# Kernel tuning notes

Hardware: AMD Instinct MI355X
Metric: run time of the kernel (lower is better)

Reference implementation:

```python
import jax, jax.numpy as jnp
import numpy as np

D_MODEL = 2048
D_COMPARE = 2048
D_MEMORY = 2048
N_HEADS = 16
KV_HEADS = 4
KV_REPEAT = N_HEADS // KV_HEADS          # 4
C_HD = D_COMPARE // N_HEADS              # 128 compare head dim
M_HD = D_MEMORY // N_HEADS               # 128 memory head dim
TOTAL_OUT = D_COMPARE + KV_HEADS * C_HD + KV_HEADS * M_HD  # 3072


def setup_inputs() -> dict:
    key = jax.random.key(0)
    ks = jax.random.split(key, 5)
    b, t = 2, 2048
    x = jax.random.normal(ks[0], (b, t, D_MODEL), dtype=jnp.float32)
    s_in = 1.0 / np.sqrt(D_MODEL)
    s_out = 1.0 / np.sqrt(D_MEMORY)
    in_w = jax.random.uniform(ks[1], (TOTAL_OUT, D_MODEL), jnp.float32, -s_in, s_in)
    in_b = jax.random.uniform(ks[2], (TOTAL_OUT,), jnp.float32, -s_in, s_in)
    out_w = jax.random.uniform(ks[3], (D_MODEL, D_MEMORY), jnp.float32, -s_out, s_out)
    out_b = jax.random.uniform(ks[4], (D_MODEL,), jnp.float32, -s_out, s_out)
    return {"x": x, "in_w": in_w, "in_b": in_b, "out_w": out_w, "out_b": out_b}


def reference(x, in_w, in_b, out_w, out_b):
    b, t, _ = x.shape
    packed = jnp.einsum("btd,od->bto", x, in_w) + in_b          # [b,t,TOTAL_OUT]
    q, k, v = jnp.split(packed, [D_COMPARE, D_COMPARE + KV_HEADS * C_HD], axis=-1)
    # q: [b, kv, rep, t, hd] -- head h maps to kv group h // KV_REPEAT
    # (torch repeat_interleave on KV head dim == grouped reshape of q heads)
    q = q.reshape(b, t, KV_HEADS, KV_REPEAT, C_HD).transpose(0, 2, 3, 1, 4)
    k = k.reshape(b, t, KV_HEADS, C_HD).transpose(0, 2, 1, 3)   # [b,kv,t,hd]
    v = v.reshape(b, t, KV_HEADS, M_HD).transpose(0, 2, 1, 3)   # [b,kv,t,mhd]
    scale = 1.0 / np.sqrt(C_HD)
    scores = jnp.einsum("bgrqd,bgkd->bgrqk", q, k) * scale      # [b,kv,rep,t,t]
    attn = jax.nn.softmax(scores, axis=-1)
    y = jnp.einsum("bgrqk,bgkd->bgrqd", attn, v)                # [b,kv,rep,t,mhd]
    y = y.transpose(0, 3, 1, 2, 4).reshape(b, t, D_MEMORY)      # heads back in order
    return jnp.einsum("btm,dm->btd", y, out_w) + out_b
```

## Files before the change

kernel.cpp:

```cpp
#include <hip/hip_runtime.h>
#include <hip/hip_bf16.h>
#include <stdint.h>

#define DEV __device__ __forceinline__

typedef __attribute__((ext_vector_type(8))) short bf16x8;
typedef __attribute__((ext_vector_type(4))) float f32x4;

DEV unsigned short f2bf(float f) {
  unsigned u = __builtin_bit_cast(unsigned, f);
  unsigned r = u + 0x7FFF + ((u >> 16) & 1);
  return (unsigned short)(r >> 16);
}

typedef __attribute__((address_space(1))) void gvoid;
typedef __attribute__((address_space(3))) void lvoid;

DEV void g2l16(const void* g, void* l) {
  __builtin_amdgcn_global_load_lds((gvoid*)g, (lvoid*)l, 16, 0, 0);
}

#define MFMA16(a, b, c) __builtin_amdgcn_mfma_f32_16x16x32_bf16(a, b, c, 0, 0, 0)

__global__ void k_cvt(const float* __restrict__ in, unsigned short* __restrict__ out, int n4) {
  int i = blockIdx.x * blockDim.x + threadIdx.x;
  int stride = gridDim.x * blockDim.x;
  for (; i < n4; i += stride) {
    float4 v = reinterpret_cast<const float4*>(in)[i];
    ushort4 o;
    o.x = f2bf(v.x); o.y = f2bf(v.y); o.z = f2bf(v.z); o.w = f2bf(v.w);
    reinterpret_cast<ushort4*>(out)[i] = o;
  }
}

template<bool BF16OUT>
__global__ __launch_bounds__(256, 2) void k_gemm(
    const unsigned short* __restrict__ A, const unsigned short* __restrict__ B,
    const float* __restrict__ bias, void* __restrict__ C,
    int M, int N, int K) {
  __shared__ unsigned short As[128 * 32];
  __shared__ unsigned short Bs[128 * 32];
  int tid = threadIdx.x;
  int lane = tid & 63, wid = tid >> 6;
  int bm = blockIdx.y * 128, bn = blockIdx.x * 128;
  int wm = (wid >> 1) * 64, wn = (wid & 1) * 64;
  int row16 = lane & 15, kq = lane >> 4;
  f32x4 acc[4][4] = {};
  int r = tid >> 2, c = (tid & 3) * 8;
  const unsigned short* Ag = A + (size_t)(bm + r) * K + c;
  const unsigned short* Bg = B + (size_t)(bn + r) * K + c;
  for (int k0 = 0; k0 < K; k0 += 32) {
    g2l16(Ag + k0, &As[tid * 8]);
    g2l16(Ag + (size_t)64 * K + k0, &As[2048 + tid * 8]);
    g2l16(Bg + k0, &Bs[tid * 8]);
    g2l16(Bg + (size_t)64 * K + k0, &Bs[2048 + tid * 8]);
    __syncthreads();
    bf16x8 a[4], b[4];
#pragma unroll
    for (int m = 0; m < 4; m++) a[m] = *(const bf16x8*)&As[(wm + m * 16 + row16) * 32 + kq * 8];
#pragma unroll
    for (int n = 0; n < 4; n++) b[n] = *(const bf16x8*)&Bs[(wn + n * 16 + row16) * 32 + kq * 8];
    __builtin_amdgcn_s_setprio(1);
#pragma unroll
    for (int m = 0; m < 4; m++)
#pragma unroll
      for (int n = 0; n < 4; n++)
        acc[m][n] = MFMA16(a[m], b[n], acc[m][n]);
    __builtin_amdgcn_s_setprio(0);
    __syncthreads();
  }
#pragma unroll
  for (int n = 0; n < 4; n++) {
    int col = bn + wn + n * 16 + row16;
    float bv = bias[col];
#pragma unroll
    for (int m = 0; m < 4; m++) {
      int rw = bm + wm + m * 16 + kq * 4;
#pragma unroll
      for (int j = 0; j < 4; j++) {
        float v = acc[m][n][j] + bv;
        if (BF16OUT) ((unsigned short*)C)[(size_t)(rw + j) * N + col] = f2bf(v);
        else         ((float*)C)[(size_t)(rw + j) * N + col] = v;
      }
    }
  }
}

__global__ void k_vt(const unsigned short* __restrict__ packed, unsigned short* __restrict__ vT) {
  __shared__ unsigned short tile[64][136];
  int g = blockIdx.y;
  int b = g >> 2, kv = g & 3;
  int t0 = blockIdx.x * 64;
  int tid = threadIdx.x;
#pragma unroll
  for (int i = 0; i < 4; i++) {
    int tl = i * 16 + (tid >> 4);
    int d0 = (tid & 15) * 8;
    bf16x8 v = *(const bf16x8*)&packed[(size_t)(b * 2048 + t0 + tl) * 3072 + 2560 + kv * 128 + d0];
    *(bf16x8*)&tile[tl][d0] = v;
  }
  __syncthreads();
  int d = tid >> 1, ts = (tid & 1) * 32;
  size_t obase = (size_t)(g * 128 + d) * 2048 + t0 + ts;
#pragma unroll
  for (int j = 0; j < 4; j++) {
    bf16x8 o;
#pragma unroll
    for (int e = 0; e < 8; e++) o[e] = (short)tile[ts + j * 8 + e][d];
    *(bf16x8*)&vT[obase + j * 8] = o;
  }
}

__global__ __launch_bounds__(256, 2) void k_flash(
    const unsigned short* __restrict__ packed,
    const unsigned short* __restrict__ vT,
    unsigned short* __restrict__ Y) {
  __shared__ unsigned short Ks[2][64 * 128];
  __shared__ unsigned short Vs[128 * 64];
  __shared__ unsigned short Ps[4][2][16 * 68];
  __shared__ float Axc[4][2][16];
  int tid = threadIdx.x, lane = tid & 63, wid = tid >> 6;
  int row16 = lane & 15, kq = lane >> 4;
  int r3 = row16 & 7;
  int g = blockIdx.x;
  int s8 = g & 7;
  int b = s8 >> 2, kv = s8 & 3;
  int w = g >> 3;
  int h = kv * 4 + (w & 3);
  int qt = w >> 2;
  size_t prow = (size_t)b * 2048;

  unsigned short* Q = &Ks[0][0];
  {
    int rr = tid >> 4;
    int cc = ((tid & 15) ^ (rr & 7)) * 8;
    const unsigned short* qg = packed + (prow + qt * 128 + rr) * 3072 + h * 128 + cc;
#pragma unroll
    for (int i = 0; i < 8; i++)
      g2l16(qg + (size_t)i * 16 * 3072, &Q[i * 2048 + tid * 8]);
  }
  asm volatile("s_waitcnt vmcnt(0)" ::: "memory");
  __builtin_amdgcn_s_barrier();
  bf16x8 q[2][4];
#pragma unroll
  for (int qi = 0; qi < 2; qi++)
#pragma unroll
    for (int kc = 0; kc < 4; kc++)
      q[qi][kc] = *(const bf16x8*)&Q[(qi * 64 + wid * 16 + row16) * 128 + (((kc * 4 + kq) ^ r3) * 8)];
  asm volatile("s_waitcnt lgkmcnt(0)" ::: "memory");
  __builtin_amdgcn_sched_barrier(0);
  __builtin_amdgcn_s_barrier();

  const unsigned short* kg0 = packed + prow * 3072 + 2048 + kv * 128;
  const unsigned short* vg0 = vT + (size_t)(b * 4 + kv) * 128 * 2048;
  int krr = tid >> 4;
  int kcc = ((tid & 15) ^ (krr & 7)) * 8;
  int vrr = tid >> 3;
  int vcc = ((tid & 7) ^ (vrr & 7)) * 8;

  auto stageK = [&](int t, int kbuf) {
    const unsigned short* kg = kg0 + (size_t)(t * 64 + krr) * 3072 + kcc;
#pragma unroll
    for (int i = 0; i < 4; i++)
      g2l16(kg + (size_t)i * 16 * 3072, &Ks[kbuf][i * 2048 + tid * 8]);
  };
  auto stageV = [&](int t) {
    const unsigned short* vg = vg0 + (size_t)vrr * 2048 + t * 64 + vcc;
#pragma unroll
    for (int i = 0; i < 4; i++)
      g2l16(vg + (size_t)i * 32 * 2048, &Vs[i * 2048 + tid * 8]);
  };

  stageK(0, 0);
  stageV(0);
  asm volatile("s_waitcnt vmcnt(4)" ::: "memory");
  __builtin_amdgcn_s_barrier();

  f32x4 o[2][8] = {};
  float mr[2] = {-1e30f, -1e30f}, lr[2] = {0.f, 0.f};
  const float sc2 = 0.08838834764831845f * 1.4426950408889634f;

  for (int t = 0; t < 32; t++) {
    int kb = t & 1;
    int tn = t < 31 ? t + 1 : 31;

    f32x4 st[2][4];
#pragma unroll
    for (int qi = 0; qi < 2; qi++)
#pragma unroll
      for (int mk = 0; mk < 4; mk++) st[qi][mk] = f32x4{0.f, 0.f, 0.f, 0.f};
#pragma unroll
    for (int mk = 0; mk < 4; mk++) {
      bf16x8 bk[4];
#pragma unroll
      for (int kc = 0; kc < 4; kc++)
        bk[kc] = *(const bf16x8*)&Ks[kb][(mk * 16 + row16) * 128 + (((kc * 4 + kq) ^ r3) * 8)];
      __builtin_amdgcn_s_setprio(1);
#pragma unroll
      for (int kc = 0; kc < 4; kc++) {
        st[0][mk] = MFMA16(bk[kc], q[0][kc], st[0][mk]);
        st[1][mk] = MFMA16(bk[kc], q[1][kc], st[1][mk]);
      }
      __builtin_amdgcn_s_setprio(0);
    }

    stageK(tn, kb ^ 1);

#pragma unroll
    for (int qi = 0; qi < 2; qi++)
#pragma unroll
      for (int mk = 0; mk < 4; mk++) st[qi][mk] *= sc2;
    float pmax[2];
#pragma unroll
    for (int qi = 0; qi < 2; qi++) {
      float p = -1e30f;
#pragma unroll
      for (int mk = 0; mk < 4; mk++)
#pragma unroll
        for (int j = 0; j < 4; j++) p = fmaxf(p, st[qi][mk][j]);
      p = fmaxf(p, __shfl_xor(p, 16));
      p = fmaxf(p, __shfl_xor(p, 32));
      pmax[qi] = p;
    }
    if (!__all(pmax[0] <= mr[0] + 8.f && pmax[1] <= mr[1] + 8.f)) {
#pragma unroll
      for (int qi = 0; qi < 2; qi++) {
        float mn = fmaxf(mr[qi], pmax[qi]);
        float al = exp2f(mr[qi] - mn);
        mr[qi] = mn;
        lr[qi] *= al;
        if (lane < 16) Axc[wid][qi][row16] = al;
      }
#pragma unroll
      for (int qi = 0; qi < 2; qi++) {
        float alo[4];
#pragma unroll
        for (int j = 0; j < 4; j++) alo[j] = Axc[wid][qi][kq * 4 + j];
#pragma unroll
        for (int np = 0; np < 8; np++)
#pragma unroll
          for (int j = 0; j < 4; j++) o[qi][np][j] *= alo[j];
      }
    }
#pragma unroll
    for (int qi = 0; qi < 2; qi++) {
      float rs = 0.f;
#pragma unroll
      for (int mk = 0; mk < 4; mk++)
#pragma unroll
        for (int j = 0; j < 4; j++) {
          st[qi][mk][j] = exp2f(st[qi][mk][j] - mr[qi]);
          rs += st[qi][mk][j];
        }
      rs += __shfl_xor(rs, 16);
      rs += __shfl_xor(rs, 32);
      lr[qi] += rs;
    }

    bf16x8 pf[2][2];
#pragma unroll
    for (int qi = 0; qi < 2; qi++) {
#pragma unroll
      for (int mk = 0; mk < 4; mk++) {
        ushort4 pw;
        pw.x = f2bf(st[qi][mk][0]); pw.y = f2bf(st[qi][mk][1]);
        pw.z = f2bf(st[qi][mk][2]); pw.w = f2bf(st[qi][mk][3]);
        *(ushort4*)&Ps[wid][qi][row16 * 68 + mk * 16 + kq * 4] = pw;
      }
#pragma unroll
      for (int k2 = 0; k2 < 2; k2++)
        pf[qi][k2] = *(const bf16x8*)&Ps[wid][qi][row16 * 68 + k2 * 32 + kq * 8];
    }

    asm volatile("s_waitcnt vmcnt(4)" ::: "memory");
    __builtin_amdgcn_s_barrier();

#pragma unroll
    for (int np = 0; np < 8; np++) {
      int vrow = np * 16 + row16;
      bf16x8 bv0 = *(const bf16x8*)&Vs[vrow * 64 + ((kq ^ r3) * 8)];
      bf16x8 bv1 = *(const bf16x8*)&Vs[vrow * 64 + (((4 + kq) ^ r3) * 8)];
      __builtin_amdgcn_s_setprio(1);
      o[0][np] = MFMA16(pf[0][0], bv0, o[0][np]);
      o[0][np] = MFMA16(pf[0][1], bv1, o[0][np]);
      o[1][np] = MFMA16(pf[1][0], bv0, o[1][np]);
      o[1][np] = MFMA16(pf[1][1], bv1, o[1][np]);
      __builtin_amdgcn_s_setprio(0);
    }

    __builtin_amdgcn_s_barrier();
    stageV(tn);
    asm volatile("s_waitcnt vmcnt(4)" ::: "memory");
    __builtin_amdgcn_s_barrier();
  }
  asm volatile("s_waitcnt vmcnt(0)" ::: "memory");

#pragma unroll
  for (int qi = 0; qi < 2; qi++)
    if (lane < 16) Axc[wid][qi][row16] = lr[qi];
#pragma unroll
  for (int qi = 0; qi < 2; qi++)
#pragma unroll
    for (int j = 0; j < 4; j++) {
      float inv = 1.f / Axc[wid][qi][kq * 4 + j];
      size_t orow = prow + (size_t)qt * 128 + qi * 64 + wid * 16 + kq * 4 + j;
#pragma unroll
      for (int np = 0; np < 8; np++)
        Y[orow * 2048 + h * 128 + np * 16 + row16] = f2bf(o[qi][np][j] * inv);
    }
}

extern "C" void kernel_launch(void* const* d_in, const int* in_sizes, int n_in,
                              void* d_out, int out_size, void* d_ws, size_t ws_size,
                              hipStream_t stream) {
  const float* x     = (const float*)d_in[0];
  const float* in_w  = (const float*)d_in[1];
  const float* in_b  = (const float*)d_in[2];
  const float* out_w = (const float*)d_in[3];
  const float* out_b = (const float*)d_in[4];
  float* out = (float*)d_out;

  unsigned short* xb     = (unsigned short*)d_ws;
  unsigned short* wb     = xb + 8388608;
  unsigned short* owb    = wb + 6291456;
  unsigned short* packed = owb + 4194304;
  unsigned short* vt     = packed + 12582912;
  unsigned short* y      = vt + 2097152;

  k_cvt<<<dim3(1024), dim3(256), 0, stream>>>(x, xb, 8388608 / 4);
  k_cvt<<<dim3(1024), dim3(256), 0, stream>>>(in_w, wb, 6291456 / 4);
  k_cvt<<<dim3(1024), dim3(256), 0, stream>>>(out_w, owb, 4194304 / 4);

  k_gemm<true><<<dim3(24, 32), dim3(256), 0, stream>>>(xb, wb, in_b, packed, 4096, 3072, 2048);
  k_vt<<<dim3(32, 8), dim3(256), 0, stream>>>(packed, vt);
  k_flash<<<dim3(512), dim3(256), 0, stream>>>(packed, vt, y);
  k_gemm<false><<<dim3(16, 32), dim3(256), 0, stream>>>(y, owb, out_b, out, 4096, 2048, 2048);
}
```

Before: 236.8 us.

## Merge conversion launches and streamline flash softmax arithmetic

Replaces the three fp32-to-bf16 conversion kernels with a single combined launch over all three buffers. In the attention kernel, the score scale is folded into an fma inside exp2, applied once to the row max instead of to every score, and the max and sum reductions are restructured as trees. It also switches the P and output bf16 conversions to the compiler's native bf16 cast, which may map to hardware conversion instructions. These cut launch overhead and VALU work in the softmax; the rounding of the native cast may differ slightly from the manual round-to-nearest-even.

```diff
diff --git a/kernel.cpp b/kernel.cpp
--- a/kernel.cpp
+++ b/kernel.cpp
@@ -13,6 +13,11 @@
   return (unsigned short)(r >> 16);
 }
 
+DEV unsigned short f2bfh(float f) {
+  __bf16 h = (__bf16)f;
+  return __builtin_bit_cast(unsigned short, h);
+}
+
 typedef __attribute__((address_space(1))) void gvoid;
 typedef __attribute__((address_space(3))) void lvoid;
 
@@ -22,14 +27,21 @@
 
 #define MFMA16(a, b, c) __builtin_amdgcn_mfma_f32_16x16x32_bf16(a, b, c, 0, 0, 0)
 
-__global__ void k_cvt(const float* __restrict__ in, unsigned short* __restrict__ out, int n4) {
+__global__ void k_cvt3(const float* __restrict__ x, unsigned short* __restrict__ xo, int nx4,
+                       const float* __restrict__ w, unsigned short* __restrict__ wo, int nw4,
+                       const float* __restrict__ v, unsigned short* __restrict__ vo, int nv4) {
   int i = blockIdx.x * blockDim.x + threadIdx.x;
   int stride = gridDim.x * blockDim.x;
-  for (; i < n4; i += stride) {
-    float4 v = reinterpret_cast<const float4*>(in)[i];
+  int tot = nx4 + nw4 + nv4;
+  for (; i < tot; i += stride) {
+    const float* src; unsigned short* dst; int j = i;
+    if (j < nx4) { src = x; dst = xo; }
+    else if ((j -= nx4) < nw4) { src = w; dst = wo; }
+    else { j -= nw4; src = v; dst = vo; }
+    float4 val = reinterpret_cast<const float4*>(src)[j];
     ushort4 o;
-    o.x = f2bf(v.x); o.y = f2bf(v.y); o.z = f2bf(v.z); o.w = f2bf(v.w);
-    reinterpret_cast<ushort4*>(out)[i] = o;
+    o.x = f2bf(val.x); o.y = f2bf(val.y); o.z = f2bf(val.z); o.w = f2bf(val.w);
+    reinterpret_cast<ushort4*>(dst)[j] = o;
   }
 }
 
@@ -206,21 +218,17 @@
 
     stageK(tn, kb ^ 1);
 
-#pragma unroll
-    for (int qi = 0; qi < 2; qi++)
-#pragma unroll
-      for (int mk = 0; mk < 4; mk++) st[qi][mk] *= sc2;
     float pmax[2];
 #pragma unroll
     for (int qi = 0; qi < 2; qi++) {
-      float p = -1e30f;
-#pragma unroll
-      for (int mk = 0; mk < 4; mk++)
-#pragma unroll
-        for (int j = 0; j < 4; j++) p = fmaxf(p, st[qi][mk][j]);
+      float a0 = fmaxf(fmaxf(st[qi][0][0], st[qi][0][1]), fmaxf(st[qi][0][2], st[qi][0][3]));
+      float a1 = fmaxf(fmaxf(st[qi][1][0], st[qi][1][1]), fmaxf(st[qi][1][2], st[qi][1][3]));
+      float a2 = fmaxf(fmaxf(st[qi][2][0], st[qi][2][1]), fmaxf(st[qi][2][2], st[qi][2][3]));
+      float a3 = fmaxf(fmaxf(st[qi][3][0], st[qi][3][1]), fmaxf(st[qi][3][2], st[qi][3][3]));
+      float p = fmaxf(fmaxf(a0, a1), fmaxf(a2, a3));
       p = fmaxf(p, __shfl_xor(p, 16));
       p = fmaxf(p, __shfl_xor(p, 32));
-      pmax[qi] = p;
+      pmax[qi] = p * sc2;
     }
     if (!__all(pmax[0] <= mr[0] + 8.f && pmax[1] <= mr[1] + 8.f)) {
 #pragma unroll
@@ -244,14 +252,17 @@
     }
 #pragma unroll
     for (int qi = 0; qi < 2; qi++) {
-      float rs = 0.f;
+      float nm = -mr[qi];
 #pragma unroll
       for (int mk = 0; mk < 4; mk++)
 #pragma unroll
-        for (int j = 0; j < 4; j++) {
-          st[qi][mk][j] = exp2f(st[qi][mk][j] - mr[qi]);
-          rs += st[qi][mk][j];
-        }
+        for (int j = 0; j < 4; j++)
+          st[qi][mk][j] = exp2f(fmaf(st[qi][mk][j], sc2, nm));
+      float s0 = (st[qi][0][0] + st[qi][0][1]) + (st[qi][0][2] + st[qi][0][3]);
+      float s1 = (st[qi][1][0] + st[qi][1][1]) + (st[qi][1][2] + st[qi][1][3]);
+      float s2 = (st[qi][2][0] + st[qi][2][1]) + (st[qi][2][2] + st[qi][2][3]);
+      float s3 = (st[qi][3][0] + st[qi][3][1]) + (st[qi][3][2] + st[qi][3][3]);
+      float rs = (s0 + s1) + (s2 + s3);
       rs += __shfl_xor(rs, 16);
       rs += __shfl_xor(rs, 32);
       lr[qi] += rs;
@@ -263,8 +274,8 @@
 #pragma unroll
       for (int mk = 0; mk < 4; mk++) {
         ushort4 pw;
-        pw.x = f2bf(st[qi][mk][0]); pw.y = f2bf(st[qi][mk][1]);
-        pw.z = f2bf(st[qi][mk][2]); pw.w = f2bf(st[qi][mk][3]);
+        pw.x = f2bfh(st[qi][mk][0]); pw.y = f2bfh(st[qi][mk][1]);
+        pw.z = f2bfh(st[qi][mk][2]); pw.w = f2bfh(st[qi][mk][3]);
         *(ushort4*)&Ps[wid][qi][row16 * 68 + mk * 16 + kq * 4] = pw;
       }
 #pragma unroll
@@ -306,7 +317,7 @@
       size_t orow = prow + (size_t)qt * 128 + qi * 64 + wid * 16 + kq * 4 + j;
 #pragma unroll
       for (int np = 0; np < 8; np++)
-        Y[orow * 2048 + h * 128 + np * 16 + row16] = f2bf(o[qi][np][j] * inv);
+        Y[orow * 2048 + h * 128 + np * 16 + row16] = f2bfh(o[qi][np][j] * inv);
     }
 }
 
@@ -327,9 +338,9 @@
   unsigned short* vt     = packed + 12582912;
   unsigned short* y      = vt + 2097152;
 
-  k_cvt<<<dim3(1024), dim3(256), 0, stream>>>(x, xb, 8388608 / 4);
-  k_cvt<<<dim3(1024), dim3(256), 0, stream>>>(in_w, wb, 6291456 / 4);
-  k_cvt<<<dim3(1024), dim3(256), 0, stream>>>(out_w, owb, 4194304 / 4);
+  k_cvt3<<<dim3(2048), dim3(256), 0, stream>>>(x, xb, 8388608 / 4,
+                                               in_w, wb, 6291456 / 4,
+                                               out_w, owb, 4194304 / 4);
 
   k_gemm<true><<<dim3(24, 32), dim3(256), 0, stream>>>(xb, wb, in_b, packed, 4096, 3072, 2048);
   k_vt<<<dim3(32, 8), dim3(256), 0, stream>>>(packed, vt);
```

New measurement: 230.0 us. -2.9%, faster.
